# Kernel tuning notes

Hardware: AMD Instinct MI355X
Metric: run time of the kernel (lower is better)

The kernel has to match this reference:

```python
import jax, jax.numpy as jnp
import numpy as np

D_MODEL = 1024
NUM_HEADS = 16
HEAD_DIM = D_MODEL // NUM_HEADS
WINDOW = 256
NEG = -1000000000.0


def setup_inputs() -> dict:
    key = jax.random.key(0)
    ks = jax.random.split(key, 9)
    B, N, D = 2, 2048, D_MODEL
    s = 1.0 / np.sqrt(D)
    inp = {
        "x": jax.random.normal(ks[0], (B, N, D), dtype=jnp.float32),
        "Wq": jax.random.normal(ks[1], (D, D), dtype=jnp.float32) * s,
        "bq": jnp.zeros((D,), dtype=jnp.float32),
        "Wk": jax.random.normal(ks[2], (D, D), dtype=jnp.float32) * s,
        "bk": jnp.zeros((D,), dtype=jnp.float32),
        "Wv": jax.random.normal(ks[3], (D, D), dtype=jnp.float32) * s,
        "bv": jnp.zeros((D,), dtype=jnp.float32),
        "Wo": jax.random.normal(ks[4], (D, D), dtype=jnp.float32) * s,
        "bo": jnp.zeros((D,), dtype=jnp.float32),
    }
    return inp


def reference(x, Wq, bq, Wk, bk, Wv, bv, Wo, bo):
    B, N, D = x.shape
    H, hd = NUM_HEADS, HEAD_DIM
    q = (x @ Wq + bq).reshape(B, N, H, hd).transpose(0, 2, 1, 3)  # [B,H,N,hd]
    k = (x @ Wk + bk).reshape(B, N, H, hd).transpose(0, 2, 1, 3)
    v = (x @ Wv + bv).reshape(B, N, H, hd).transpose(0, 2, 1, 3)

    i = jnp.arange(N)[:, None]
    j = jnp.arange(N)[None, :]
    blocked = (j > i) | (j < i - WINDOW)  # causal + local window
    mask = jnp.where(blocked, jnp.float32(NEG), jnp.float32(0.0))  # [N,N]

    logits = jnp.einsum("bhid,bhjd->bhij", q, k) / jnp.sqrt(jnp.float32(hd))
    logits = logits + mask[None, None, :, :]
    attn = jax.nn.softmax(logits, axis=-1)
    out = jnp.einsum("bhij,bhjd->bhid", attn, v)  # [B,H,N,hd]
    out = out.transpose(0, 2, 1, 3).reshape(B, N, D)
    return out @ Wo + bo
```

## Files before the change

kernel.cpp:

```cpp
#include <hip/hip_runtime.h>


typedef unsigned short ushort_t;
typedef __bf16 bf16x8 __attribute__((ext_vector_type(8)));
typedef float f32x4 __attribute__((ext_vector_type(4)));
typedef unsigned short ushort8 __attribute__((ext_vector_type(8)));

#define LOG2E 1.4426950408889634f

static __device__ __forceinline__ ushort_t f2b(float f) {
    union { float f; unsigned int u; } x;
    x.f = f;
    unsigned int u = x.u;
    unsigned int r = (u + 0x7FFFu + ((u >> 16) & 1u)) >> 16;
    return (ushort_t)r;
}

static __device__ __forceinline__ void store_out(float* p, float v) { *p = v; }
static __device__ __forceinline__ void store_out(ushort_t* p, float v) { *p = f2b(v); }

static __device__ __forceinline__ int sw(int row, int c) {
    return (row * 8 + (c ^ (row & 7))) * 8;
}

static __device__ __forceinline__ void gload_lds16(const ushort_t* g, ushort_t* l) {
    __builtin_amdgcn_global_load_lds(
        (const __attribute__((address_space(1))) void*)g,
        (__attribute__((address_space(3))) void*)l, 16, 0, 0);
}

__global__ __launch_bounds__(256) void prep_kernel(
    const float* __restrict__ x, ushort_t* __restrict__ xbf,
    const float* __restrict__ W0, const float* __restrict__ W1,
    const float* __restrict__ W2, const float* __restrict__ W3,
    ushort_t* __restrict__ T0, ushort_t* __restrict__ T1,
    ushort_t* __restrict__ T2, ushort_t* __restrict__ T3) {
    int tx = threadIdx.x, ty = threadIdx.y;
    if (blockIdx.z == 4) {
        int idx = (blockIdx.y * 32 + blockIdx.x) * 256 + ty * 32 + tx;
        int i = idx * 16;
#pragma unroll
        for (int half = 0; half < 2; half++) {
            f32x4 a = *(const f32x4*)&x[i + half * 8];
            f32x4 b = *(const f32x4*)&x[i + half * 8 + 4];
            ushort8 o;
#pragma unroll
            for (int e = 0; e < 4; e++) o[e] = f2b(a[e]);
#pragma unroll
            for (int e = 0; e < 4; e++) o[4 + e] = f2b(b[e]);
            *(ushort8*)&xbf[i + half * 8] = o;
        }
        return;
    }
    __shared__ ushort_t tile[32][33];
    const float* W;
    ushort_t* T;
    switch (blockIdx.z) {
        case 0: W = W0; T = T0; break;
        case 1: W = W1; T = T1; break;
        case 2: W = W2; T = T2; break;
        default: W = W3; T = T3; break;
    }
    int xx = blockIdx.x * 32 + tx;
    int ybase = blockIdx.y * 32 + ty;
#pragma unroll
    for (int r = 0; r < 4; r++) tile[ty + r * 8][tx] = f2b(W[(ybase + r * 8) * 1024 + xx]);
    __syncthreads();
    int xo = blockIdx.y * 32 + tx;
    int yobase = blockIdx.x * 32 + ty;
#pragma unroll
    for (int r = 0; r < 4; r++) T[(yobase + r * 8) * 1024 + xo] = tile[tx][ty + r * 8];
}

__global__ __launch_bounds__(256) void gemm_qkv_kernel(
    const ushort_t* __restrict__ A,
    const ushort_t* __restrict__ Bt0, const ushort_t* __restrict__ Bt1,
    const ushort_t* __restrict__ Bt2,
    const float* __restrict__ bias0, const float* __restrict__ bias1,
    const float* __restrict__ bias2,
    ushort_t* __restrict__ C0, ushort_t* __restrict__ C1, ushort_t* __restrict__ C2,
    float os0, float os1, float os2) {
    __shared__ ushort_t Al[64 * 64];
    __shared__ ushort_t Bl[128 * 64];

    const int id = blockIdx.x;
    const int xcd = id & 7;
    const int s = id >> 3;
    int m_blk = (xcd >> 1) * 16 + (s & 15);
    int ncol = (xcd & 1) * 12 + (s >> 4);
    int zsel = ncol >> 3;
    ncol &= 7;
    const int m0 = m_blk * 64;
    const int n0 = ncol * 128;

    const ushort_t* Bt;
    const float* bias;
    ushort_t* C;
    float oscale;
    if (zsel == 0) { Bt = Bt0; bias = bias0; C = C0; oscale = os0; }
    else if (zsel == 1) { Bt = Bt1; bias = bias1; C = C1; oscale = os1; }
    else { Bt = Bt2; bias = bias2; C = C2; oscale = os2; }

    const int tid = threadIdx.x;
    const int w = tid >> 6;
    const int l = tid & 63;
    const int wm = (w >> 1) * 32;
    const int wn = (w & 1) * 64;
    const int lrow = l & 15;
    const int lq = l >> 4;

    f32x4 acc[2][4];
#pragma unroll
    for (int mi = 0; mi < 2; mi++)
#pragma unroll
        for (int ni = 0; ni < 4; ni++) acc[mi][ni] = 0.0f;

    const int kt0 = (id * 5) & 15;
    for (int it = 0; it < 16; it++) {
        const int kt = ((kt0 + it) & 15) * 64;
#pragma unroll
        for (int t = 0; t < 2; t++) {
            int idx = t * 256 + tid;
            int row = idx >> 3, cs = idx & 7, c = cs ^ (row & 7);
            gload_lds16(&A[(long)(m0 + row) * 1024 + kt + c * 8], &Al[idx * 8]);
        }
#pragma unroll
        for (int t = 0; t < 4; t++) {
            int idx = t * 256 + tid;
            int row = idx >> 3, cs = idx & 7, c = cs ^ (row & 7);
            gload_lds16(&Bt[(long)(n0 + row) * 1024 + kt + c * 8], &Bl[idx * 8]);
        }
        __syncthreads();
#pragma unroll
        for (int ks = 0; ks < 64; ks += 32) {
            const int cb = (ks >> 3) + lq;
            bf16x8 af[2], bfr[4];
#pragma unroll
            for (int mi = 0; mi < 2; mi++)
                af[mi] = *(const bf16x8*)&Al[sw(wm + mi * 16 + lrow, cb)];
#pragma unroll
            for (int ni = 0; ni < 4; ni++)
                bfr[ni] = *(const bf16x8*)&Bl[sw(wn + ni * 16 + lrow, cb)];
#pragma unroll
            for (int mi = 0; mi < 2; mi++)
#pragma unroll
                for (int ni = 0; ni < 4; ni++)
                    acc[mi][ni] = __builtin_amdgcn_mfma_f32_16x16x32_bf16(
                        af[mi], bfr[ni], acc[mi][ni], 0, 0, 0);
        }
        __syncthreads();
    }

#pragma unroll
    for (int ni = 0; ni < 4; ni++) {
        int n = n0 + wn + ni * 16 + lrow;
        float bv = bias[n];
#pragma unroll
        for (int mi = 0; mi < 2; mi++) {
#pragma unroll
            for (int r = 0; r < 4; r++) {
                int m = m0 + wm + mi * 16 + lq * 4 + r;
                store_out(&C[(long)m * 1024 + n], (acc[mi][ni][r] + bv) * oscale);
            }
        }
    }
}

__global__ __launch_bounds__(256) void gemm_out_kernel(
    const ushort_t* __restrict__ A, const ushort_t* __restrict__ Bt,
    const float* __restrict__ bias, float* __restrict__ C) {
    __shared__ ushort_t Al[64 * 64];
    __shared__ ushort_t Bl[128 * 64];

    const int id = blockIdx.x;
    const int xcd = id & 7;
    const int s = id >> 3;
    const int m_blk = xcd * 8 + (s & 7);
    const int ncol = s >> 3;
    const int m0 = m_blk * 64;
    const int n0 = ncol * 128;

    const int tid = threadIdx.x;
    const int w = tid >> 6;
    const int l = tid & 63;
    const int wm = (w >> 1) * 32;
    const int wn = (w & 1) * 64;
    const int lrow = l & 15;
    const int lq = l >> 4;

    f32x4 acc[2][4];
#pragma unroll
    for (int mi = 0; mi < 2; mi++)
#pragma unroll
        for (int ni = 0; ni < 4; ni++) acc[mi][ni] = 0.0f;

    const int kt0 = (id * 5) & 15;
    for (int it = 0; it < 16; it++) {
        const int kt = ((kt0 + it) & 15) * 64;
#pragma unroll
        for (int t = 0; t < 2; t++) {
            int idx = t * 256 + tid;
            int row = idx >> 3, cs = idx & 7, c = cs ^ (row & 7);
            gload_lds16(&A[(long)(m0 + row) * 1024 + kt + c * 8], &Al[idx * 8]);
        }
#pragma unroll
        for (int t = 0; t < 4; t++) {
            int idx = t * 256 + tid;
            int row = idx >> 3, cs = idx & 7, c = cs ^ (row & 7);
            gload_lds16(&Bt[(long)(n0 + row) * 1024 + kt + c * 8], &Bl[idx * 8]);
        }
        __syncthreads();
#pragma unroll
        for (int ks = 0; ks < 64; ks += 32) {
            const int cb = (ks >> 3) + lq;
            bf16x8 af[2], bfr[4];
#pragma unroll
            for (int mi = 0; mi < 2; mi++)
                af[mi] = *(const bf16x8*)&Al[sw(wm + mi * 16 + lrow, cb)];
#pragma unroll
            for (int ni = 0; ni < 4; ni++)
                bfr[ni] = *(const bf16x8*)&Bl[sw(wn + ni * 16 + lrow, cb)];
#pragma unroll
            for (int mi = 0; mi < 2; mi++)
#pragma unroll
                for (int ni = 0; ni < 4; ni++)
                    acc[mi][ni] = __builtin_amdgcn_mfma_f32_16x16x32_bf16(
                        af[mi], bfr[ni], acc[mi][ni], 0, 0, 0);
        }
        __syncthreads();
    }

#pragma unroll
    for (int ni = 0; ni < 4; ni++) {
        int n = n0 + wn + ni * 16 + lrow;
        float bv = bias[n];
#pragma unroll
        for (int mi = 0; mi < 2; mi++) {
#pragma unroll
            for (int r = 0; r < 4; r++) {
                int m = m0 + wm + mi * 16 + lq * 4 + r;
                C[(long)m * 1024 + n] = acc[mi][ni][r] + bv;
            }
        }
    }
}

__global__ __launch_bounds__(256) void attn_kernel(
    const ushort_t* __restrict__ Q, const ushort_t* __restrict__ K,
    const ushort_t* __restrict__ V, ushort_t* __restrict__ O) {
    __shared__ ushort_t Kl[128 * 64];
    __shared__ ushort_t Vt[64 * 136];
    __shared__ ushort_t Pb[4 * 16 * 40];

    const int id = blockIdx.x;
    const int xcd = id & 7;
    const int s = id >> 3;
    const int bh = xcd * 4 + (s >> 5);
    const int b = bh >> 4;
    const int h = bh & 15;
    const int i0 = (s & 31) * 64;

    const int tid = threadIdx.x;
    const int w = tid >> 6;
    const int l = tid & 63;
    const int lrow = l & 15;
    const int lq = l >> 4;
    const int q0 = i0 + w * 16;

    const long baseBH = ((long)b * 2048) * 1024 + (long)h * 64;

    const ushort_t* qrow = Q + baseBH + (long)(q0 + lrow) * 1024;
    bf16x8 aq0 = *(const bf16x8*)&qrow[lq * 8];
    bf16x8 aq1 = *(const bf16x8*)&qrow[32 + lq * 8];

    float lpart[4];
    f32x4 oacc[4];
#pragma unroll
    for (int r = 0; r < 4; r++) lpart[r] = 0.0f;
#pragma unroll
    for (int ni = 0; ni < 4; ni++) oacc[ni] = 0.0f;

    const int kstart = (i0 - 256) > 0 ? (i0 - 256) : 0;
    const int kend = i0 + 64;
    ushort_t* Pw = &Pb[w * 16 * 40];

    for (int cs = kstart; cs < kend; cs += 128) {
        const int ce = (cs + 128 < kend) ? cs + 128 : kend;
        const int rows = ce - cs;
#pragma unroll
        for (int t = 0; t < 4; t++) {
            int idx = t * 256 + tid;
            int rr = idx >> 3;
            int cc = idx & 7;
            int c = cc ^ (rr & 7);
            int key = cs + rr;
            key = key < 2047 ? key : 2047;
            gload_lds16(&K[baseBH + (long)key * 1024 + c * 8], &Kl[idx * 8]);
        }
        {
            int rr = tid >> 1;
            int ch = (tid & 1) * 32;
            if (rr < rows) {
                const ushort_t* vrow = V + baseBH + (long)(cs + rr) * 1024 + ch;
#pragma unroll
                for (int g = 0; g < 4; g++) {
                    ushort8 vv = *(const ushort8*)&vrow[g * 8];
#pragma unroll
                    for (int e = 0; e < 8; e++) Vt[(ch + g * 8 + e) * 136 + rr] = vv[e];
                }
            }
        }
        __syncthreads();

        for (int kb = cs; kb < ce; kb += 32) {
            if (kb > q0 + 15 || kb + 31 < q0 - 256) continue;
            const int rb = kb - cs;
            f32x4 S0 = 0.0f, S1 = 0.0f;
            {
                bf16x8 bk;
                bk = *(const bf16x8*)&Kl[sw(rb + lrow, lq)];
                S0 = __builtin_amdgcn_mfma_f32_16x16x32_bf16(aq0, bk, S0, 0, 0, 0);
                bk = *(const bf16x8*)&Kl[sw(rb + lrow, 4 + lq)];
                S0 = __builtin_amdgcn_mfma_f32_16x16x32_bf16(aq1, bk, S0, 0, 0, 0);
                bk = *(const bf16x8*)&Kl[sw(rb + 16 + lrow, lq)];
                S1 = __builtin_amdgcn_mfma_f32_16x16x32_bf16(aq0, bk, S1, 0, 0, 0);
                bk = *(const bf16x8*)&Kl[sw(rb + 16 + lrow, 4 + lq)];
                S1 = __builtin_amdgcn_mfma_f32_16x16x32_bf16(aq1, bk, S1, 0, 0, 0);
            }
            const int col0 = kb + lrow;
            const int col1 = kb + 16 + lrow;
#pragma unroll
            for (int r = 0; r < 4; r++) {
                const int i = q0 + lq * 4 + r;
                float p0 = (col0 > i || col0 < i - 256) ? 0.0f : exp2f(S0[r] * LOG2E);
                float p1 = (col1 > i || col1 < i - 256) ? 0.0f : exp2f(S1[r] * LOG2E);
                lpart[r] += p0 + p1;
                const int prow = lq * 4 + r;
                Pw[prow * 40 + lrow] = f2b(p0);
                Pw[prow * 40 + 16 + lrow] = f2b(p1);
            }
            bf16x8 pf = *(const bf16x8*)&Pw[lrow * 40 + lq * 8];
#pragma unroll
            for (int ni = 0; ni < 4; ni++) {
                bf16x8 vf = *(const bf16x8*)&Vt[(ni * 16 + lrow) * 136 + rb + lq * 8];
                oacc[ni] = __builtin_amdgcn_mfma_f32_16x16x32_bf16(pf, vf, oacc[ni], 0, 0, 0);
            }
        }
        __syncthreads();
    }

    float lS[4];
#pragma unroll
    for (int r = 0; r < 4; r++) {
        float rs = lpart[r];
#pragma unroll
        for (int off = 8; off; off >>= 1) rs += __shfl_xor(rs, off, 64);
        lS[r] = rs;
    }

#pragma unroll
    for (int ni = 0; ni < 4; ni++) {
#pragma unroll
        for (int r = 0; r < 4; r++) {
            const int i = q0 + lq * 4 + r;
            const int d = ni * 16 + lrow;
            O[baseBH + (long)i * 1024 + d] = f2b(oacc[ni][r] / lS[r]);
        }
    }
}

extern "C" void kernel_launch(void* const* d_in, const int* in_sizes, int n_in,
                              void* d_out, int out_size, void* d_ws, size_t ws_size,
                              hipStream_t stream) {
    const float* x  = (const float*)d_in[0];
    const float* Wq = (const float*)d_in[1];
    const float* bq = (const float*)d_in[2];
    const float* Wk = (const float*)d_in[3];
    const float* bk = (const float*)d_in[4];
    const float* Wv = (const float*)d_in[5];
    const float* bv = (const float*)d_in[6];
    const float* Wo = (const float*)d_in[7];
    const float* bo = (const float*)d_in[8];
    float* out = (float*)d_out;

    ushort_t* ws = (ushort_t*)d_ws;
    const size_t WMAT = (size_t)1024 * 1024;
    const size_t ACT = (size_t)2 * 2048 * 1024;
    ushort_t* xbf = ws;
    ushort_t* Wqt = xbf + ACT;
    ushort_t* Wkt = Wqt + WMAT;
    ushort_t* Wvt = Wkt + WMAT;
    ushort_t* Wot = Wvt + WMAT;
    ushort_t* qws = Wot + WMAT;
    ushort_t* kws = qws + ACT;
    ushort_t* vws = kws + ACT;
    ushort_t* aws = xbf;

    prep_kernel<<<dim3(32, 32, 5), dim3(32, 8), 0, stream>>>(
        x, xbf, Wq, Wk, Wv, Wo, Wqt, Wkt, Wvt, Wot);

    gemm_qkv_kernel<<<1536, 256, 0, stream>>>(
        xbf, Wqt, Wkt, Wvt, bq, bk, bv, qws, kws, vws, 0.125f, 1.0f, 1.0f);

    attn_kernel<<<1024, 256, 0, stream>>>(qws, kws, vws, aws);

    gemm_out_kernel<<<512, 256, 0, stream>>>(aws, Wot, bo, out);
}
```

Baseline: 162.5 us.

## Store V transposed from projection GEMM and load it via direct-to-LDS copies

The V projection GEMM now writes its output in a head-major transposed layout ([h*64+d][b*2048+n]) with vectorized 4-element bf16 stores. The attention kernel can then fetch V tiles with swizzled global-to-LDS 16-byte loads, the same way it fetches K. This removes the per-thread scalar transpose scatter into shared memory, which caused many small LDS writes and bank conflicts. The cost is strided column-wise global stores in the GEMM epilogue, and a clamp on the key index near the sequence end.

Result: no change. 163.1 us (+0.3%).

```diff
diff --git a/kernel.cpp b/kernel.cpp
--- a/kernel.cpp
+++ b/kernel.cpp
@@ -5,6 +5,7 @@
 typedef __bf16 bf16x8 __attribute__((ext_vector_type(8)));
 typedef float f32x4 __attribute__((ext_vector_type(4)));
 typedef unsigned short ushort8 __attribute__((ext_vector_type(8)));
+typedef unsigned short ushort4v __attribute__((ext_vector_type(4)));
 
 #define LOG2E 1.4426950408889634f
 
@@ -151,16 +152,32 @@
         __syncthreads();
     }
 
-#pragma unroll
-    for (int ni = 0; ni < 4; ni++) {
-        int n = n0 + wn + ni * 16 + lrow;
-        float bv = bias[n];
-#pragma unroll
-        for (int mi = 0; mi < 2; mi++) {
-#pragma unroll
-            for (int r = 0; r < 4; r++) {
-                int m = m0 + wm + mi * 16 + lq * 4 + r;
-                store_out(&C[(long)m * 1024 + n], (acc[mi][ni][r] + bv) * oscale);
+    if (zsel == 2) {
+#pragma unroll
+        for (int ni = 0; ni < 4; ni++) {
+            int n = n0 + wn + ni * 16 + lrow;
+            float bv = bias[n];
+#pragma unroll
+            for (int mi = 0; mi < 2; mi++) {
+                int m = m0 + wm + mi * 16 + lq * 4;
+                ushort4v o;
+#pragma unroll
+                for (int r = 0; r < 4; r++) o[r] = f2b((acc[mi][ni][r] + bv) * oscale);
+                *(ushort4v*)&C[(long)n * 4096 + m] = o;
+            }
+        }
+    } else {
+#pragma unroll
+        for (int ni = 0; ni < 4; ni++) {
+            int n = n0 + wn + ni * 16 + lrow;
+            float bv = bias[n];
+#pragma unroll
+            for (int mi = 0; mi < 2; mi++) {
+#pragma unroll
+                for (int r = 0; r < 4; r++) {
+                    int m = m0 + wm + mi * 16 + lq * 4 + r;
+                    store_out(&C[(long)m * 1024 + n], (acc[mi][ni][r] + bv) * oscale);
+                }
             }
         }
     }
@@ -247,9 +264,9 @@
 
 __global__ __launch_bounds__(256) void attn_kernel(
     const ushort_t* __restrict__ Q, const ushort_t* __restrict__ K,
-    const ushort_t* __restrict__ V, ushort_t* __restrict__ O) {
+    const ushort_t* __restrict__ VT, ushort_t* __restrict__ O) {
     __shared__ ushort_t Kl[128 * 64];
-    __shared__ ushort_t Vt[64 * 136];
+    __shared__ ushort_t Vtl[64 * 128];
     __shared__ ushort_t Pb[4 * 16 * 40];
 
     const int id = blockIdx.x;
@@ -268,6 +285,7 @@
     const int q0 = i0 + w * 16;
 
     const long baseBH = ((long)b * 2048) * 1024 + (long)h * 64;
+    const long baseVT = (long)h * 64 * 4096 + (long)b * 2048;
 
     const ushort_t* qrow = Q + baseBH + (long)(q0 + lrow) * 1024;
     bf16x8 aq0 = *(const bf16x8*)&qrow[lq * 8];
@@ -286,7 +304,6 @@
 
     for (int cs = kstart; cs < kend; cs += 128) {
         const int ce = (cs + 128 < kend) ? cs + 128 : kend;
-        const int rows = ce - cs;
 #pragma unroll
         for (int t = 0; t < 4; t++) {
             int idx = t * 256 + tid;
@@ -297,18 +314,15 @@
             key = key < 2047 ? key : 2047;
             gload_lds16(&K[baseBH + (long)key * 1024 + c * 8], &Kl[idx * 8]);
         }
-        {
-            int rr = tid >> 1;
-            int ch = (tid & 1) * 32;
-            if (rr < rows) {
-                const ushort_t* vrow = V + baseBH + (long)(cs + rr) * 1024 + ch;
-#pragma unroll
-                for (int g = 0; g < 4; g++) {
-                    ushort8 vv = *(const ushort8*)&vrow[g * 8];
-#pragma unroll
-                    for (int e = 0; e < 8; e++) Vt[(ch + g * 8 + e) * 136 + rr] = vv[e];
-                }
-            }
+#pragma unroll
+        for (int t = 0; t < 4; t++) {
+            int idx = t * 256 + tid;
+            int rr = idx >> 4;
+            int cc = idx & 15;
+            int c = (cc & 8) | ((cc & 7) ^ (rr & 7));
+            int kc = cs + c * 8;
+            kc = kc < 2040 ? kc : 2040;
+            gload_lds16(&VT[baseVT + (long)rr * 4096 + kc], &Vtl[idx * 8]);
         }
         __syncthreads();
 
@@ -342,7 +356,9 @@
             bf16x8 pf = *(const bf16x8*)&Pw[lrow * 40 + lq * 8];
 #pragma unroll
             for (int ni = 0; ni < 4; ni++) {
-                bf16x8 vf = *(const bf16x8*)&Vt[(ni * 16 + lrow) * 136 + rb + lq * 8];
+                int ccg = (rb >> 3) + lq;
+                int rsw = (ccg & 8) | ((ccg & 7) ^ (lrow & 7));
+                bf16x8 vf = *(const bf16x8*)&Vtl[(ni * 16 + lrow) * 128 + rsw * 8];
                 oacc[ni] = __builtin_amdgcn_mfma_f32_16x16x32_bf16(pf, vf, oacc[ni], 0, 0, 0);
             }
         }
```
